# Performance work log

Measured on AMD Instinct MI355X. Metric: run time of the kernel, lower is better.

The kernel has to match this reference:

```python
import jax, jax.numpy as jnp
import numpy as np

N = 50000   # nodes
E = 400000  # edges
G = 256     # graphs in batch
D = 256     # out_dim (scalar channel width)
VD = 16     # vector channel width after v_emb


def setup_inputs() -> dict:
    key = jax.random.key(0)
    ks = jax.random.split(key, 12)

    def rn(k, shape, scale=0.02):
        return (jax.random.normal(k, shape) * scale).astype(jnp.float32)

    return dict(
        node_s=jax.random.normal(ks[0], (N, 23), jnp.float32),
        node_v=jax.random.normal(ks[1], (N, 4, 3), jnp.float32),
        edge_s=jax.random.normal(ks[2], (E, 17), jnp.float32),
        edge_index=jax.random.randint(ks[3], (2, E), 0, N, jnp.int32),
        batch=jnp.sort(jax.random.randint(ks[4], (N,), 0, G, jnp.int32)),
        Ws=rn(ks[5], (23, D)), bs=jnp.zeros((D,), jnp.float32),
        Wv=rn(ks[6], (4, VD)), bv=jnp.zeros((VD,), jnp.float32),
        We=rn(ks[7], (18, D)), be=jnp.zeros((D,), jnp.float32),
        Wm1=rn(ks[8], (2 * D + VD + D, D)), bm1=jnp.zeros((D,), jnp.float32),
        Wm2=rn(ks[9], (D, D)), bm2=jnp.zeros((D,), jnp.float32),
        Wn=rn(ks[10], (D + VD, D)), bn=jnp.zeros((D,), jnp.float32),
        gamma=jnp.ones((D,), jnp.float32), beta=jnp.zeros((D,), jnp.float32),
    )


def reference(node_s, node_v, edge_s, edge_index, batch,
              Ws, bs, Wv, bv, We, be, Wm1, bm1, Wm2, bm2, Wn, bn, gamma, beta):
    # --- embeddings ---
    s = node_s @ Ws + bs                                            # [N, D]
    e_in = jnp.concatenate([edge_s, jnp.zeros((edge_s.shape[0], 1), edge_s.dtype)], axis=-1)  # no edge_v branch
    e = e_in @ We + be                                              # [E, D]
    # v_emb: Linear over the 4 vector channels -> [N, VD, 3]
    v = jnp.einsum('nkc,ko->noc', node_v, Wv) + bv[None, :, None]
    v_norm = jnp.linalg.norm(v, axis=-1)                            # [N, VD]

    # --- SimpleGVPConv: gather -> 2-layer MLP per edge -> scatter-mean ---
    src, dst = edge_index[0], edge_index[1]                         # PyG: s_j = s[src], s_i = s[dst]
    m_in = jnp.concatenate([s[dst], s[src], v_norm[src], e], axis=-1)  # [E, 2D+VD+D]
    m = jax.nn.relu(m_in @ Wm1 + bm1) @ Wm2 + bm2                   # [E, D]
    agg = jax.ops.segment_sum(m, dst, num_segments=N)               # [N, D]
    cnt = jax.ops.segment_sum(jnp.ones((E,), m.dtype), dst, num_segments=N)
    s = s + agg / jnp.maximum(cnt, 1.0)[:, None]                    # mean aggr + residual update

    # --- node MLP: Linear -> LayerNorm -> ReLU (dropout = eval identity) ---
    feat = jnp.concatenate([s, v_norm], axis=-1)                    # [N, D+VD]
    h = feat @ Wn + bn                                              # [N, D]
    mu = h.mean(axis=-1, keepdims=True)
    var = h.var(axis=-1, keepdims=True)
    h = (h - mu) * jax.lax.rsqrt(var + 1e-5) * gamma + beta
    h = jax.nn.relu(h)

    # --- global mean pool ---
    gsum = jax.ops.segment_sum(h, batch, num_segments=G)            # [G, D]
    gcnt = jax.ops.segment_sum(jnp.ones((h.shape[0],), h.dtype), batch, num_segments=G)
    return gsum / jnp.maximum(gcnt, 1.0)[:, None]
```

## Files before the change

kernel.cpp:

```cpp
#include <hip/hip_runtime.h>
#include <hip/hip_bf16.h>

typedef unsigned short u16;
typedef __attribute__((ext_vector_type(8))) short short8;
typedef __attribute__((ext_vector_type(4))) short short4v;
typedef __attribute__((ext_vector_type(4))) float f32x4;

#define NN 50000
#define EE 400000
#define GG 256
#define MP 50048
#define KS 64
#define K2 320
#define EWS 260
#define EAGB 4096
#define NSEG 32
#define SEGSZ 1563

static __device__ __forceinline__ __hip_bfloat16 f2b(float x) { return __float2bfloat16(x); }
static __device__ __forceinline__ float u16tof(u16 v) {
    unsigned x = ((unsigned)v) << 16;
    float f;
    __builtin_memcpy(&f, &x, 4);
    return f;
}
static __device__ __forceinline__ u16 ftou16(float x) {
    __hip_bfloat16 h = __float2bfloat16(x);
    u16 b;
    __builtin_memcpy(&b, &h, 2);
    return b;
}

static __device__ __forceinline__ float dot256(const float* __restrict__ a,
                                               const float* __restrict__ b, int c) {
    const float* __restrict__ bp = b + c;
    float s0 = 0.f, s1 = 0.f, s2 = 0.f, s3 = 0.f;
    float s4 = 0.f, s5 = 0.f, s6 = 0.f, s7 = 0.f;
#pragma unroll 4
    for (int j = 0; j < 256; j += 8) {
        s0 += a[j]     * bp[(size_t)(j)     * 256];
        s1 += a[j + 1] * bp[(size_t)(j + 1) * 256];
        s2 += a[j + 2] * bp[(size_t)(j + 2) * 256];
        s3 += a[j + 3] * bp[(size_t)(j + 3) * 256];
        s4 += a[j + 4] * bp[(size_t)(j + 4) * 256];
        s5 += a[j + 5] * bp[(size_t)(j + 5) * 256];
        s6 += a[j + 6] * bp[(size_t)(j + 6) * 256];
        s7 += a[j + 7] * bp[(size_t)(j + 7) * 256];
    }
    return ((s0 + s1) + (s2 + s3)) + ((s4 + s5) + (s6 + s7));
}

__global__ __launch_bounds__(256) void phase1(const float* __restrict__ Wm1,
                                              const float* __restrict__ Wn,
                                              const float* __restrict__ Wm2,
                                              const float* __restrict__ We,
                                              const float* __restrict__ be,
                                              const float* __restrict__ bm1,
                                              const float* __restrict__ bm2,
                                              const float* __restrict__ Ws,
                                              const float* __restrict__ bs,
                                              __hip_bfloat16* __restrict__ W1pqT,
                                              __hip_bfloat16* __restrict__ W2T,
                                              float* __restrict__ Wc, float* __restrict__ bc,
                                              float* __restrict__ crow,
                                              const float* __restrict__ node_s,
                                              const float* __restrict__ node_v,
                                              const float* __restrict__ Wv,
                                              const float* __restrict__ bv,
                                              __hip_bfloat16* __restrict__ XL2,
                                              const int* __restrict__ ei,
                                              const int* __restrict__ batch,
                                              int* __restrict__ cnt,
                                              int* __restrict__ gstart) {
    int blk = blockIdx.x, tid = threadIdx.x;
    if (blk < 4) {
        int c0 = blk * 128;
        int w = tid >> 6, lane = tid & 63;
        int quad = lane >> 4, l16 = lane & 15;
        f32x4 acc[4][2] = {};
        for (int jt = 0; jt < 256; jt += 32) {
            int j0 = jt + quad * 8;
            short8 af[4], bf[2];
#pragma unroll
            for (int mi = 0; mi < 4; ++mi) {
                int k = mi * 16 + l16;
                const float* ar = nullptr;
                if (k < 23) ar = Ws + (size_t)k * 256;
                else if (k == 39) ar = bs;
                float v0 = 0.f, v1 = 0.f, v2 = 0.f, v3 = 0.f, v4 = 0.f, v5 = 0.f, v6 = 0.f, v7 = 0.f;
                if (ar) {
                    f32x4 x0 = *(const f32x4*)(ar + j0);
                    f32x4 x1 = *(const f32x4*)(ar + j0 + 4);
                    v0 = x0[0]; v1 = x0[1]; v2 = x0[2]; v3 = x0[3];
                    v4 = x1[0]; v5 = x1[1]; v6 = x1[2]; v7 = x1[3];
                }
                af[mi][0] = (short)ftou16(v0); af[mi][1] = (short)ftou16(v1);
                af[mi][2] = (short)ftou16(v2); af[mi][3] = (short)ftou16(v3);
                af[mi][4] = (short)ftou16(v4); af[mi][5] = (short)ftou16(v5);
                af[mi][6] = (short)ftou16(v6); af[mi][7] = (short)ftou16(v7);
            }
#pragma unroll
            for (int ni = 0; ni < 2; ++ni) {
                int c = c0 + w * 32 + ni * 16 + l16;
                const float* Wm1h = (c < 256) ? Wm1 : (Wm1 + 256 * 256);
                int cc = c & 255;
#pragma unroll
                for (int u = 0; u < 8; ++u)
                    bf[ni][u] = (short)ftou16(Wm1h[(size_t)(j0 + u) * 256 + cc]);
            }
#pragma unroll
            for (int mi = 0; mi < 4; ++mi) {
#pragma unroll
                for (int ni = 0; ni < 2; ++ni)
                    acc[mi][ni] = __builtin_amdgcn_mfma_f32_16x16x32_bf16(af[mi], bf[ni], acc[mi][ni], 0, 0, 0);
            }
        }
#pragma unroll
        for (int mi = 0; mi < 4; ++mi) {
#pragma unroll
            for (int ni = 0; ni < 2; ++ni) {
                int c = c0 + w * 32 + ni * 16 + l16;
#pragma unroll
                for (int r = 0; r < 4; ++r) {
                    int k = mi * 16 + quad * 4 + r;
                    float v = acc[mi][ni][r];
                    if (k >= 23 && k < 39)
                        v = (c >= 256) ? Wm1[(size_t)(512 + (k - 23)) * 256 + (c & 255)] : 0.f;
                    W1pqT[(size_t)c * KS + k] = f2b(v);
                }
            }
        }
    } else if (blk < 14) {
        int wb = blk - 4;
        int kt0 = (wb >> 1) * 64;
        int c0 = (wb & 1) * 128;
        int w = tid >> 6, lane = tid & 63;
        int quad = lane >> 4, l16 = lane & 15;
        f32x4 acc[4][2] = {};
        for (int jt = 0; jt < 256; jt += 32) {
            int j0 = jt + quad * 8;
            short8 af[4], bf[2];
#pragma unroll
            for (int mi = 0; mi < 4; ++mi) {
                int k = kt0 + mi * 16 + l16;
                const float* ar = nullptr;
                if (k < 23) ar = Ws + (size_t)k * 256;
                else if (k == 39) ar = bs;
                else if (k >= 40 && k < 296) ar = Wm2 + (size_t)(k - 40) * 256;
                float v0 = 0.f, v1 = 0.f, v2 = 0.f, v3 = 0.f, v4 = 0.f, v5 = 0.f, v6 = 0.f, v7 = 0.f;
                if (ar) {
                    f32x4 x0 = *(const f32x4*)(ar + j0);
                    f32x4 x1 = *(const f32x4*)(ar + j0 + 4);
                    v0 = x0[0]; v1 = x0[1]; v2 = x0[2]; v3 = x0[3];
                    v4 = x1[0]; v5 = x1[1]; v6 = x1[2]; v7 = x1[3];
                }
                af[mi][0] = (short)ftou16(v0); af[mi][1] = (short)ftou16(v1);
                af[mi][2] = (short)ftou16(v2); af[mi][3] = (short)ftou16(v3);
                af[mi][4] = (short)ftou16(v4); af[mi][5] = (short)ftou16(v5);
                af[mi][6] = (short)ftou16(v6); af[mi][7] = (short)ftou16(v7);
            }
#pragma unroll
            for (int ni = 0; ni < 2; ++ni) {
                int c = c0 + w * 32 + ni * 16 + l16;
#pragma unroll
                for (int u = 0; u < 8; ++u)
                    bf[ni][u] = (short)ftou16(Wn[(size_t)(j0 + u) * 256 + c]);
            }
#pragma unroll
            for (int mi = 0; mi < 4; ++mi) {
#pragma unroll
                for (int ni = 0; ni < 2; ++ni)
                    acc[mi][ni] = __builtin_amdgcn_mfma_f32_16x16x32_bf16(af[mi], bf[ni], acc[mi][ni], 0, 0, 0);
            }
        }
#pragma unroll
        for (int mi = 0; mi < 4; ++mi) {
#pragma unroll
            for (int ni = 0; ni < 2; ++ni) {
                int c = c0 + w * 32 + ni * 16 + l16;
#pragma unroll
                for (int r = 0; r < 4; ++r) {
                    int k = kt0 + mi * 16 + quad * 4 + r;
                    float v = acc[mi][ni][r];
                    if (k >= 23 && k < 39) v = Wn[(size_t)(256 + k - 23) * 256 + c];
                    W2T[(size_t)c * K2 + k] = f2b(v);
                }
            }
        }
    } else if (blk < 33) {
        int b = blk - 14, c = tid;
        if (b < 17) Wc[b * 256 + c] = dot256(&We[b * 256], &Wm1[528 * 256], c);
        else if (b == 17) bc[c] = bm1[c] + dot256(be, &Wm1[528 * 256], c);
        else crow[c] = dot256(bm2, Wn, c);
    } else if (blk < 12533) {
        int w = tid >> 6, lane = tid & 63;
        int n = (blk - 33) * 4 + w;
        if (n < NN) {
            float lv = (lane < 23) ? node_s[(size_t)n * 23 + lane] : 0.f;
            float vv = (lane < 12) ? node_v[(size_t)n * 12 + lane] : 0.f;
            float nvk[12];
#pragma unroll
            for (int k = 0; k < 12; ++k) nvk[k] = __shfl(vv, k, 64);
            float vn = 0.f;
            if (lane < 16) {
                float b0 = bv[lane];
                float vx = b0, vy = b0, vz = b0;
#pragma unroll
                for (int k = 0; k < 4; ++k) {
                    float wv = Wv[k * 16 + lane];
                    vx += nvk[k * 3 + 0] * wv;
                    vy += nvk[k * 3 + 1] * wv;
                    vz += nvk[k * 3 + 2] * wv;
                }
                vn = sqrtf(vx * vx + vy * vy + vz * vz);
            }
            int vsrc = (lane >= 23 && lane < 39) ? (lane - 23) : 0;
            float vbc = __shfl(vn, vsrc, 64);
            float outv;
            if (lane < 23) outv = lv;
            else if (lane < 39) outv = vbc;
            else if (lane == 39) outv = 1.f;
            else outv = 0.f;
            __hip_bfloat16* row = XL2 + (size_t)n * K2;
            row[lane] = f2b(outv);
            if (lane < 24) row[296 + lane] = f2b(0.f);
        }
    } else if (blk < 14096) {
        int e = (blk - 12533) * 256 + tid;
        if (e < EE) atomicAdd(&cnt[ei[EE + e]], 1);
    } else {
        int n = (blk - 14096) * 256 + tid;
        if (n < NN) {
            int bn = batch[n];
            int bp = (n == 0) ? -1 : batch[n - 1];
            for (int g = bp + 1; g <= bn; ++g) gstart[g] = n;
            if (n == NN - 1)
                for (int g = bn + 1; g <= GG; ++g) gstart[g] = NN;
        }
    }
}

__global__ __launch_bounds__(256) void scan1(const int* __restrict__ cnt, int* __restrict__ rowptr,
                                             int* __restrict__ bsum) {
    int tid = threadIdx.x, i = blockIdx.x * 256 + tid;
    __shared__ int sd[256];
    int v = (i < NN) ? cnt[i] : 0;
    sd[tid] = v;
    __syncthreads();
    for (int off = 1; off < 256; off <<= 1) {
        int t = (tid >= off) ? sd[tid - off] : 0;
        __syncthreads();
        sd[tid] += t;
        __syncthreads();
    }
    if (i < NN) rowptr[i] = sd[tid] - v;
    if (tid == 255) bsum[blockIdx.x] = sd[255];
}
__global__ __launch_bounds__(256) void scan2(int* __restrict__ bsum, const int* __restrict__ gstart,
                                             float* __restrict__ ginv, int* __restrict__ qc) {
    int c = threadIdx.x;
    __shared__ int sd[256];
    int v = (c < 196) ? bsum[c] : 0;
    sd[c] = v;
    __syncthreads();
    for (int off = 1; off < 256; off <<= 1) {
        int t = (c >= off) ? sd[c - off] : 0;
        __syncthreads();
        sd[c] += t;
        __syncthreads();
    }
    if (c < 196) bsum[c] = sd[c] - v;
    ginv[c] = 1.f / fmaxf((float)(gstart[c + 1] - gstart[c]), 1.f);
    if (c < NSEG) qc[c * 64] = c * SEGSZ + (EAGB / NSEG);
}
__global__ __launch_bounds__(256) void scan3(const int* __restrict__ cnt, const int* __restrict__ bsum,
                                             int* __restrict__ rowptr, int* __restrict__ cursor) {
    int i = blockIdx.x * 256 + threadIdx.x;
    if (i < NN) {
        int v = rowptr[i] + bsum[blockIdx.x];
        rowptr[i] = v;
        cursor[i] = v;
        if (i == NN - 1) rowptr[NN] = v + cnt[i];
    }
}

__global__ __launch_bounds__(256, 2) void gemm1_fill(const u16* __restrict__ A, const u16* __restrict__ Bt,
                                                     __hip_bfloat16* __restrict__ C,
                                                     const int* __restrict__ ei, int* __restrict__ cursor,
                                                     int* __restrict__ eid, int* __restrict__ srcv,
                                                     const float* __restrict__ Wc,
                                                     u16* __restrict__ WcBf) {
    __shared__ __align__(16) u16 At[128 * 64];
    __shared__ __align__(16) u16 Bs[128 * 64];
    int blk = blockIdx.x, tid = threadIdx.x;
    if (blk >= 1564) {
        if (blk == 3127) {
            for (int idx = tid; idx < 8192; idx += 256) {
                int ni = idx >> 9;
                int l = (idx >> 3) & 63;
                int j = idx & 7;
                int k = ((l >> 4) << 3) + j;
                int c = ni * 16 + (l & 15);
                float v = (k < 17) ? Wc[k * 256 + c] : 0.f;
                WcBf[idx] = ftou16(v);
            }
            return;
        }
        int e = (blk - 1564) * 256 + tid;
        if (e < EE) {
            int d = ei[EE + e];
            int s = ei[e];
            int pos = atomicAdd(&cursor[d], 1);
            eid[pos] = e;
            srcv[pos] = s;
        }
        return;
    }
    long m0 = (long)(blk >> 2) * 128;
    long n0 = (long)(blk & 3) * 128;
    int wid = tid >> 6, lane = tid & 63;
    int wm = wid >> 1, wn = wid & 1;
    int quad = lane >> 4, l16 = lane & 15;
    f32x4 acc[4][4] = {};
    int r0 = tid >> 3;
    int cc = (tid & 7) * 8;
    const u16* Ab = A + (m0 + r0) * K2 + cc;
    const u16* Bb = Bt + (n0 + r0) * KS + cc;
#pragma unroll
    for (int i = 0; i < 4; ++i) {
        int row = r0 + i * 32;
        __builtin_amdgcn_global_load_lds(
            (const __attribute__((address_space(1))) void*)(Ab + (long)(i * 32) * K2),
            (__attribute__((address_space(3))) void*)(&At[row * 64 + cc]), 16, 0, 0);
    }
#pragma unroll
    for (int i = 0; i < 4; ++i) {
        int row = r0 + i * 32;
        __builtin_amdgcn_global_load_lds(
            (const __attribute__((address_space(1))) void*)(Bb + (long)(i * 32) * KS),
            (__attribute__((address_space(3))) void*)(&Bs[row * 64 + cc]), 16, 0, 0);
    }
    __syncthreads();
#pragma unroll
    for (int kk = 0; kk < 64; kk += 32) {
        short8 af[4], bf[4];
#pragma unroll
        for (int mi = 0; mi < 4; ++mi)
            af[mi] = *(const short8*)&At[(wm * 64 + mi * 16 + l16) * 64 + kk + quad * 8];
#pragma unroll
        for (int ni = 0; ni < 4; ++ni)
            bf[ni] = *(const short8*)&Bs[(wn * 64 + ni * 16 + l16) * 64 + kk + quad * 8];
#pragma unroll
        for (int mi = 0; mi < 4; ++mi) {
#pragma unroll
            for (int ni = 0; ni < 4; ++ni)
                acc[mi][ni] = __builtin_amdgcn_mfma_f32_16x16x32_bf16(af[mi], bf[ni], acc[mi][ni], 0, 0, 0);
        }
    }
#pragma unroll
    for (int mi = 0; mi < 4; ++mi) {
#pragma unroll
        for (int ni = 0; ni < 4; ++ni) {
            long row = m0 + wm * 64 + mi * 16 + quad * 4;
            long col = n0 + wn * 64 + ni * 16 + l16;
#pragma unroll
            for (int r = 0; r < 4; ++r)
                C[(row + r) * 512 + col] = f2b(acc[mi][ni][r]);
        }
    }
}

__global__ __launch_bounds__(64) void edge_agg(const u16* __restrict__ PQ,
                                               const float* __restrict__ edge_s,
                                               const int* __restrict__ srcv,
                                               const int* __restrict__ eid,
                                               const int* __restrict__ rowptr,
                                               const u16* __restrict__ WcBf,
                                               const float* __restrict__ bc,
                                               int* __restrict__ qc,
                                               __hip_bfloat16* __restrict__ XL2) {
    __shared__ __align__(16) u16 EW[16 * EWS];
    int lane = threadIdx.x;
    int l16 = lane & 15, quad = lane >> 4;
    int seg = blockIdx.x & (NSEG - 1);
    int send = seg * SEGSZ + SEGSZ;
    if (send > NN) send = NN;
    int* segc = qc + seg * 64;
    short8 wcf[16];
#pragma unroll
    for (int ni = 0; ni < 16; ++ni)
        wcf[ni] = *(const short8*)&WcBf[ni * 512 + lane * 8];
    f32x4 bc4 = *(const f32x4*)&bc[lane * 4];
    const f32x4 zf = {0.f, 0.f, 0.f, 0.f};
    int n = seg * SEGSZ + (blockIdx.x >> 5);
    int st = rowptr[n], en = rowptr[n + 1];
    int ee = 0, ss = 0;
    {
        int m0 = en - st;
        if (m0 > 64) m0 = 64;
        if (lane < m0) {
            ee = eid[st + lane];
            ss = srcv[st + lane];
        }
    }
    short4v p4 = *(const short4v*)&PQ[(size_t)n * 512 + lane * 4];
    while (true) {
        int nn = 0;
        if (lane == 0) nn = atomicAdd(segc, 1);
        nn = __builtin_amdgcn_readfirstlane(nn);
        int stN = 0, enN = 0, eeN = 0, ssN = 0;
        short4v p4N = {0, 0, 0, 0};
        if (nn < send) {
            stN = rowptr[nn];
            enN = rowptr[nn + 1];
            int mN = enN - stN;
            if (mN > 64) mN = 64;
            if (lane < mN) {
                eeN = eid[stN + lane];
                ssN = srcv[stN + lane];
            }
            p4N = *(const short4v*)&PQ[(size_t)nn * 512 + lane * 4];
        }
        int deg = en - st;
        f32x4 pb;
#pragma unroll
        for (int i = 0; i < 4; ++i) pb[i] = u16tof((u16)p4[i]) + bc4[i];
        f32x4 acc = {0.f, 0.f, 0.f, 0.f};
        for (int base = 0; base < deg; base += 64) {
            int m = deg - base;
            if (m > 64) m = 64;
            int mm1 = m - 1;
            if (base > 0) {
                ee = 0; ss = 0;
                if (lane < m) {
                    ee = eid[st + base + lane];
                    ss = srcv[st + base + lane];
                }
            }
            auto loadQ = [&](int p) {
                int pc = (p < mm1) ? p : mm1;
                int s = __builtin_amdgcn_readlane(ss, pc);
                return *(const short4v*)&PQ[(size_t)s * 512 + 256 + lane * 4];
            };
            int ng = (m + 15) >> 4;
            for (int g = 0; g < ng; ++g) {
                int b16 = g * 16;
                short4v qA0 = loadQ(b16 + 0);
                short4v qA1 = loadQ(b16 + 1);
                short4v qA2 = loadQ(b16 + 2);
                short4v qA3 = loadQ(b16 + 3);
                short4v qA4 = loadQ(b16 + 4);
                short4v qA5 = loadQ(b16 + 5);
                short4v qA6 = loadQ(b16 + 6);
                short4v qA7 = loadQ(b16 + 7);
                int li = b16 + l16;
                if (li > mm1) li = mm1;
                int ev = __shfl(ee, li, 64);
                const float* ep = edge_s + (size_t)ev * 17 + quad * 8;
                float a0 = 0.f, a1 = 0.f, a2 = 0.f, a3 = 0.f, a4 = 0.f, a5 = 0.f, a6 = 0.f, a7 = 0.f;
                if (quad < 2) {
                    a0 = ep[0]; a1 = ep[1]; a2 = ep[2]; a3 = ep[3];
                    a4 = ep[4]; a5 = ep[5]; a6 = ep[6]; a7 = ep[7];
                } else if (quad == 2) {
                    a0 = ep[0];
                }
                short8 af;
                af[0] = (short)ftou16(a0); af[1] = (short)ftou16(a1);
                af[2] = (short)ftou16(a2); af[3] = (short)ftou16(a3);
                af[4] = (short)ftou16(a4); af[5] = (short)ftou16(a5);
                af[6] = (short)ftou16(a6); af[7] = (short)ftou16(a7);
#pragma unroll
                for (int ni = 0; ni < 16; ++ni) {
                    f32x4 ew = __builtin_amdgcn_mfma_f32_16x16x32_bf16(af, wcf[ni], zf, 0, 0, 0);
#pragma unroll
                    for (int r = 0; r < 4; ++r)
                        EW[(quad * 4 + r) * EWS + ni * 16 + l16] = ftou16(ew[r]);
                }
                int mg = m - b16;
                if (mg > 16) mg = 16;
                short4v qB0 = {0, 0, 0, 0}, qB1 = {0, 0, 0, 0}, qB2 = {0, 0, 0, 0}, qB3 = {0, 0, 0, 0};
                short4v qB4 = {0, 0, 0, 0}, qB5 = {0, 0, 0, 0}, qB6 = {0, 0, 0, 0}, qB7 = {0, 0, 0, 0};
                if (mg > 8) {
                    qB0 = loadQ(b16 + 8);
                    qB1 = loadQ(b16 + 9);
                    qB2 = loadQ(b16 + 10);
                    qB3 = loadQ(b16 + 11);
                    qB4 = loadQ(b16 + 12);
                    qB5 = loadQ(b16 + 13);
                    qB6 = loadQ(b16 + 14);
                    qB7 = loadQ(b16 + 15);
                }
#define CONSUME(QQ, c)                                                              \
                {                                                                   \
                    int jj = (c);                                                   \
                    if (jj < mg) {                                                  \
                        short4v ew4 = *(const short4v*)&EW[jj * EWS + lane * 4];    \
                        _Pragma("unroll")                                           \
                        for (int i = 0; i < 4; ++i)                                 \
                            acc[i] += fmaxf(pb[i] + u16tof((u16)QQ[i]) +            \
                                            u16tof((u16)ew4[i]), 0.f);              \
                    }                                                               \
                }
                CONSUME(qA0, 0)  CONSUME(qA1, 1)  CONSUME(qA2, 2)  CONSUME(qA3, 3)
                CONSUME(qA4, 4)  CONSUME(qA5, 5)  CONSUME(qA6, 6)  CONSUME(qA7, 7)
                CONSUME(qB0, 8)  CONSUME(qB1, 9)  CONSUME(qB2, 10) CONSUME(qB3, 11)
                CONSUME(qB4, 12) CONSUME(qB5, 13) CONSUME(qB6, 14) CONSUME(qB7, 15)
#undef CONSUME
            }
        }
        float inv = 1.f / fmaxf((float)deg, 1.f);
        short4v ov;
#pragma unroll
        for (int i = 0; i < 4; ++i) ov[i] = (short)ftou16(acc[i] * inv);
        *(short4v*)&XL2[(size_t)n * K2 + 40 + lane * 4] = ov;
        if (nn >= send) break;
        n = nn;
        st = stN; en = enN;
        ee = eeN; ss = ssN;
        p4 = p4N;
    }
}

__global__ __launch_bounds__(256, 2) void gemm2_lnp(const u16* __restrict__ A, const u16* __restrict__ Bt,
                                                    const int* __restrict__ cnt, const int* __restrict__ batch,
                                                    const float* __restrict__ bn, const float* __restrict__ crow,
                                                    const float* __restrict__ gamma, const float* __restrict__ beta,
                                                    const float* __restrict__ ginv, float* __restrict__ out) {
    __shared__ __align__(16) u16 At[64 * 64];
    __shared__ __align__(16) u16 Bs[256 * 64];
    __shared__ float rsum[4][64], rsum2[4][64];
    __shared__ int sdeg[64], sbatch[64];
    int tid = threadIdx.x;
    long m0 = (long)blockIdx.x * 64;
    int w = tid >> 6, lane = tid & 63;
    int quad = lane >> 4, l16 = lane & 15;
    f32x4 acc[4][4] = {};
    int r0 = tid >> 3;
    int cc = (tid & 7) * 8;
    const u16* Ab = A + (m0 + r0) * K2 + cc;
    const u16* Bb = Bt + (long)r0 * K2 + cc;
    for (int kt = 0; kt < K2; kt += 64) {
#pragma unroll
        for (int i = 0; i < 2; ++i) {
            int row = r0 + i * 32;
            __builtin_amdgcn_global_load_lds(
                (const __attribute__((address_space(1))) void*)(Ab + (long)(i * 32) * K2 + kt),
                (__attribute__((address_space(3))) void*)(&At[row * 64 + cc]), 16, 0, 0);
        }
#pragma unroll
        for (int i = 0; i < 8; ++i) {
            int row = r0 + i * 32;
            __builtin_amdgcn_global_load_lds(
                (const __attribute__((address_space(1))) void*)(Bb + (long)(i * 32) * K2 + kt),
                (__attribute__((address_space(3))) void*)(&Bs[row * 64 + cc]), 16, 0, 0);
        }
        __syncthreads();
#pragma unroll
        for (int kk = 0; kk < 64; kk += 32) {
            short8 af[4], bf[4];
#pragma unroll
            for (int mi = 0; mi < 4; ++mi)
                af[mi] = *(const short8*)&At[(mi * 16 + l16) * 64 + kk + quad * 8];
#pragma unroll
            for (int ni = 0; ni < 4; ++ni)
                bf[ni] = *(const short8*)&Bs[(w * 64 + ni * 16 + l16) * 64 + kk + quad * 8];
#pragma unroll
            for (int mi = 0; mi < 4; ++mi) {
#pragma unroll
                for (int ni = 0; ni < 4; ++ni)
                    acc[mi][ni] = __builtin_amdgcn_mfma_f32_16x16x32_bf16(af[mi], bf[ni], acc[mi][ni], 0, 0, 0);
            }
        }
        __syncthreads();
    }
    if (tid < 64) {
        long n = m0 + tid;
        sdeg[tid] = (n < NN) ? cnt[n] : 0;
        sbatch[tid] = (n < NN) ? batch[n] : -1;
    }
    __syncthreads();
    float bn_l[4], cr_l[4], g_l[4], be_l[4];
#pragma unroll
    for (int ni = 0; ni < 4; ++ni) {
        int col = w * 64 + ni * 16 + l16;
        bn_l[ni] = bn[col];
        cr_l[ni] = crow[col];
        g_l[ni] = gamma[col];
        be_l[ni] = beta[col];
    }
#pragma unroll
    for (int mi = 0; mi < 4; ++mi) {
#pragma unroll
        for (int r = 0; r < 4; ++r) {
            int row = mi * 16 + quad * 4 + r;
            float cr_on = (sdeg[row] > 0) ? 1.f : 0.f;
            float s = 0.f, s2 = 0.f;
#pragma unroll
            for (int ni = 0; ni < 4; ++ni) {
                float xv = acc[mi][ni][r] + bn_l[ni] + cr_on * cr_l[ni];
                acc[mi][ni][r] = xv;
                s += xv;
                s2 += xv * xv;
            }
            s += __shfl_xor(s, 1, 64);  s2 += __shfl_xor(s2, 1, 64);
            s += __shfl_xor(s, 2, 64);  s2 += __shfl_xor(s2, 2, 64);
            s += __shfl_xor(s, 4, 64);  s2 += __shfl_xor(s2, 4, 64);
            s += __shfl_xor(s, 8, 64);  s2 += __shfl_xor(s2, 8, 64);
            if (l16 == 0) { rsum[w][row] = s; rsum2[w][row] = s2; }
        }
    }
    __syncthreads();
    float mu_a[4][4], rs_a[4][4];
#pragma unroll
    for (int mi = 0; mi < 4; ++mi) {
#pragma unroll
        for (int r = 0; r < 4; ++r) {
            int row = mi * 16 + quad * 4 + r;
            float S = rsum[0][row] + rsum[1][row] + rsum[2][row] + rsum[3][row];
            float S2 = rsum2[0][row] + rsum2[1][row] + rsum2[2][row] + rsum2[3][row];
            float mu = S * (1.f / 256.f);
            mu_a[mi][r] = mu;
            rs_a[mi][r] = rsqrtf(S2 * (1.f / 256.f) - mu * mu + 1e-5f);
        }
    }
#pragma unroll
    for (int ni = 0; ni < 4; ++ni) {
        int col = w * 64 + ni * 16 + l16;
        float pacc = 0.f;
        int curg = -1;
#pragma unroll
        for (int mi = 0; mi < 4; ++mi) {
#pragma unroll
            for (int r = 0; r < 4; ++r) {
                int row = mi * 16 + quad * 4 + r;
                int g = sbatch[row];
                float y = (acc[mi][ni][r] - mu_a[mi][r]) * rs_a[mi][r] * g_l[ni] + be_l[ni];
                y = fmaxf(y, 0.f);
                if (g != curg) {
                    if (curg >= 0) atomicAdd(&out[curg * 256 + col], pacc * ginv[curg]);
                    pacc = 0.f;
                    curg = g;
                }
                if (g >= 0) pacc += y;
            }
        }
        if (curg >= 0) atomicAdd(&out[curg * 256 + col], pacc * ginv[curg]);
    }
}

extern "C" void kernel_launch(void* const* d_in, const int* in_sizes, int n_in,
                              void* d_out, int out_size, void* d_ws, size_t ws_size,
                              hipStream_t stream) {
    const float* node_s = (const float*)d_in[0];
    const float* node_v = (const float*)d_in[1];
    const float* edge_s = (const float*)d_in[2];
    const int* ei = (const int*)d_in[3];
    const int* batch = (const int*)d_in[4];
    const float* Ws = (const float*)d_in[5];
    const float* bs = (const float*)d_in[6];
    const float* Wv = (const float*)d_in[7];
    const float* bv = (const float*)d_in[8];
    const float* We = (const float*)d_in[9];
    const float* be = (const float*)d_in[10];
    const float* Wm1 = (const float*)d_in[11];
    const float* bm1 = (const float*)d_in[12];
    const float* Wm2 = (const float*)d_in[13];
    const float* bm2 = (const float*)d_in[14];
    const float* Wn = (const float*)d_in[15];
    const float* bn = (const float*)d_in[16];
    const float* gamma = (const float*)d_in[17];
    const float* beta = (const float*)d_in[18];

    char* ws = (char*)d_ws;
    size_t off = 0;
    auto take = [&](size_t n) {
        void* p = ws + off;
        off = (off + n + 255) & ~(size_t)255;
        return p;
    };
    __hip_bfloat16* XL2 = (__hip_bfloat16*)take((size_t)MP * K2 * 2);
    __hip_bfloat16* PQ = (__hip_bfloat16*)take((size_t)MP * 512 * 2);
    __hip_bfloat16* W1pqT = (__hip_bfloat16*)take(512 * KS * 2);
    __hip_bfloat16* W2T = (__hip_bfloat16*)take(256 * K2 * 2);
    float* Wc = (float*)take(17 * 256 * 4);
    float* bc = (float*)take(256 * 4);
    float* crow = (float*)take(256 * 4);
    u16* WcBf = (u16*)take(16 * 512 * 2);
    int* cnt = (int*)take(NN * 4);
    int* gstart = (int*)take((GG + 1) * 4);
    float* ginv = (float*)take(GG * 4);
    int* rowptr = (int*)take((NN + 1) * 4);
    int* cursor = (int*)take(NN * 4);
    int* eid = (int*)take(EE * 4);
    int* srcv = (int*)take(EE * 4);
    int* bsum = (int*)take(256 * 4);
    int* qc = (int*)take(NSEG * 64 * 4);

    hipMemsetAsync(cnt, 0, NN * 4, stream);
    hipMemsetAsync(d_out, 0, (size_t)out_size * 4, stream);

    phase1<<<14292, 256, 0, stream>>>(Wm1, Wn, Wm2, We, be, bm1, bm2, Ws, bs,
                                      W1pqT, W2T, Wc, bc, crow,
                                      node_s, node_v, Wv, bv, XL2, ei, batch, cnt, gstart);

    scan1<<<196, 256, 0, stream>>>(cnt, rowptr, bsum);
    scan2<<<1, 256, 0, stream>>>(bsum, gstart, ginv, qc);
    scan3<<<196, 256, 0, stream>>>(cnt, bsum, rowptr, cursor);

    gemm1_fill<<<3128, 256, 0, stream>>>((const u16*)XL2, (const u16*)W1pqT, PQ, ei, cursor, eid,
                                         srcv, Wc, WcBf);

    edge_agg<<<EAGB, 64, 0, stream>>>((const u16*)PQ, edge_s, srcv, eid, rowptr, WcBf, bc, qc, XL2);

    gemm2_lnp<<<782, 256, 0, stream>>>((const u16*)XL2, (const u16*)W2T, cnt, batch,
                                       bn, crow, gamma, beta, ginv, (float*)d_out);
}
```

Measured before the change: 293.5 us.

## Process two destination nodes per wave in edge aggregation to overlap gathers

The edge-aggregation kernel now claims two consecutive nodes per atomic work grab, and each wave prefetches row data for both. When both nodes have degree at most 16, all Q-row gathers and edge-feature loads for both nodes are issued before the MFMA and consume phases, so more memory requests are in flight per wave. Higher-degree pairs fall back to the original per-node path, and the initial work-queue offset is doubled to match the two-node stride. This raises register pressure from the 32 extra short4 gather buffers, which may reduce occupancy or cause spills.

After: 313.3 us. 1.07x slower.

```diff
diff --git a/kernel.cpp b/kernel.cpp
--- a/kernel.cpp
+++ b/kernel.cpp
@@ -271,7 +271,7 @@
     }
     if (c < 196) bsum[c] = sd[c] - v;
     ginv[c] = 1.f / fmaxf((float)(gstart[c + 1] - gstart[c]), 1.f);
-    if (c < NSEG) qc[c * 64] = c * SEGSZ + (EAGB / NSEG);
+    if (c < NSEG) qc[c * 64] = c * SEGSZ + 2 * (EAGB / NSEG);
 }
 __global__ __launch_bounds__(256) void scan3(const int* __restrict__ cnt, const int* __restrict__ bsum,
                                              int* __restrict__ rowptr, int* __restrict__ cursor) {
@@ -392,35 +392,43 @@
         wcf[ni] = *(const short8*)&WcBf[ni * 512 + lane * 8];
     f32x4 bc4 = *(const f32x4*)&bc[lane * 4];
     const f32x4 zf = {0.f, 0.f, 0.f, 0.f};
-    int n = seg * SEGSZ + (blockIdx.x >> 5);
-    int st = rowptr[n], en = rowptr[n + 1];
-    int ee = 0, ss = 0;
-    {
-        int m0 = en - st;
-        if (m0 > 64) m0 = 64;
-        if (lane < m0) {
-            ee = eid[st + lane];
-            ss = srcv[st + lane];
-        }
-    }
-    short4v p4 = *(const short4v*)&PQ[(size_t)n * 512 + lane * 4];
-    while (true) {
-        int nn = 0;
-        if (lane == 0) nn = atomicAdd(segc, 1);
-        nn = __builtin_amdgcn_readfirstlane(nn);
-        int stN = 0, enN = 0, eeN = 0, ssN = 0;
-        short4v p4N = {0, 0, 0, 0};
-        if (nn < send) {
-            stN = rowptr[nn];
-            enN = rowptr[nn + 1];
-            int mN = enN - stN;
-            if (mN > 64) mN = 64;
-            if (lane < mN) {
-                eeN = eid[stN + lane];
-                ssN = srcv[stN + lane];
-            }
-            p4N = *(const short4v*)&PQ[(size_t)nn * 512 + lane * 4];
-        }
+
+    auto buildAf = [&](int ee, int mm1) {
+        int li = l16;
+        if (li > mm1) li = mm1;
+        int ev = __shfl(ee, li, 64);
+        const float* ep = edge_s + (size_t)ev * 17 + quad * 8;
+        float a0 = 0.f, a1 = 0.f, a2 = 0.f, a3 = 0.f, a4 = 0.f, a5 = 0.f, a6 = 0.f, a7 = 0.f;
+        if (quad < 2) {
+            a0 = ep[0]; a1 = ep[1]; a2 = ep[2]; a3 = ep[3];
+            a4 = ep[4]; a5 = ep[5]; a6 = ep[6]; a7 = ep[7];
+        } else if (quad == 2) {
+            a0 = ep[0];
+        }
+        short8 af;
+        af[0] = (short)ftou16(a0); af[1] = (short)ftou16(a1);
+        af[2] = (short)ftou16(a2); af[3] = (short)ftou16(a3);
+        af[4] = (short)ftou16(a4); af[5] = (short)ftou16(a5);
+        af[6] = (short)ftou16(a6); af[7] = (short)ftou16(a7);
+        return af;
+    };
+    auto mfmaToEW = [&](short8 af) {
+#pragma unroll
+        for (int ni = 0; ni < 16; ++ni) {
+            f32x4 ew = __builtin_amdgcn_mfma_f32_16x16x32_bf16(af, wcf[ni], zf, 0, 0, 0);
+#pragma unroll
+            for (int r = 0; r < 4; ++r)
+                EW[(quad * 4 + r) * EWS + ni * 16 + l16] = ftou16(ew[r]);
+        }
+    };
+    auto storeN = [&](int n, f32x4 acc, int deg) {
+        float inv = 1.f / fmaxf((float)deg, 1.f);
+        short4v ov;
+#pragma unroll
+        for (int i = 0; i < 4; ++i) ov[i] = (short)ftou16(acc[i] * inv);
+        *(short4v*)&XL2[(size_t)n * K2 + 40 + lane * 4] = ov;
+    };
+    auto processGeneral = [&](int n, int st, int en, int ee, int ss, short4v p4) {
         int deg = en - st;
         f32x4 pb;
 #pragma unroll
@@ -469,13 +477,7 @@
                 af[2] = (short)ftou16(a2); af[3] = (short)ftou16(a3);
                 af[4] = (short)ftou16(a4); af[5] = (short)ftou16(a5);
                 af[6] = (short)ftou16(a6); af[7] = (short)ftou16(a7);
-#pragma unroll
-                for (int ni = 0; ni < 16; ++ni) {
-                    f32x4 ew = __builtin_amdgcn_mfma_f32_16x16x32_bf16(af, wcf[ni], zf, 0, 0, 0);
-#pragma unroll
-                    for (int r = 0; r < 4; ++r)
-                        EW[(quad * 4 + r) * EWS + ni * 16 + l16] = ftou16(ew[r]);
-                }
+                mfmaToEW(af);
                 int mg = m - b16;
                 if (mg > 16) mg = 16;
                 short4v qB0 = {0, 0, 0, 0}, qB1 = {0, 0, 0, 0}, qB2 = {0, 0, 0, 0}, qB3 = {0, 0, 0, 0};
@@ -508,16 +510,156 @@
 #undef CONSUME
             }
         }
-        float inv = 1.f / fmaxf((float)deg, 1.f);
-        short4v ov;
-#pragma unroll
-        for (int i = 0; i < 4; ++i) ov[i] = (short)ftou16(acc[i] * inv);
-        *(short4v*)&XL2[(size_t)n * K2 + 40 + lane * 4] = ov;
-        if (nn >= send) break;
-        n = nn;
-        st = stN; en = enN;
-        ee = eeN; ss = ssN;
-        p4 = p4N;
+        storeN(n, acc, deg);
+    };
+
+    int nA = seg * SEGSZ + 2 * (blockIdx.x >> 5);
+    int nB = nA + 1;
+    bool vB = nB < send;
+    int stA = rowptr[nA], enA = rowptr[nA + 1];
+    int eeA = 0, ssA = 0;
+    {
+        int m0 = enA - stA;
+        if (m0 > 64) m0 = 64;
+        if (lane < m0) {
+            eeA = eid[stA + lane];
+            ssA = srcv[stA + lane];
+        }
+    }
+    short4v p4A = *(const short4v*)&PQ[(size_t)nA * 512 + lane * 4];
+    int stB = 0, enB = 0, eeB = 0, ssB = 0;
+    short4v p4B = {0, 0, 0, 0};
+    if (vB) {
+        stB = rowptr[nB];
+        enB = rowptr[nB + 1];
+        int m0 = enB - stB;
+        if (m0 > 64) m0 = 64;
+        if (lane < m0) {
+            eeB = eid[stB + lane];
+            ssB = srcv[stB + lane];
+        }
+        p4B = *(const short4v*)&PQ[(size_t)nB * 512 + lane * 4];
+    }
+    while (true) {
+        int nnA = 0;
+        if (lane == 0) nnA = atomicAdd(segc, 2);
+        nnA = __builtin_amdgcn_readfirstlane(nnA);
+        int nnB = nnA + 1;
+        int stNA = 0, enNA = 0, eeNA = 0, ssNA = 0;
+        int stNB = 0, enNB = 0, eeNB = 0, ssNB = 0;
+        short4v p4NA = {0, 0, 0, 0}, p4NB = {0, 0, 0, 0};
+        if (nnA < send) {
+            stNA = rowptr[nnA];
+            enNA = rowptr[nnA + 1];
+            int mN = enNA - stNA;
+            if (mN > 64) mN = 64;
+            if (lane < mN) {
+                eeNA = eid[stNA + lane];
+                ssNA = srcv[stNA + lane];
+            }
+            p4NA = *(const short4v*)&PQ[(size_t)nnA * 512 + lane * 4];
+        }
+        if (nnB < send) {
+            stNB = rowptr[nnB];
+            enNB = rowptr[nnB + 1];
+            int mN = enNB - stNB;
+            if (mN > 64) mN = 64;
+            if (lane < mN) {
+                eeNB = eid[stNB + lane];
+                ssNB = srcv[stNB + lane];
+            }
+            p4NB = *(const short4v*)&PQ[(size_t)nnB * 512 + lane * 4];
+        }
+        int degA = enA - stA;
+        int degB = vB ? (enB - stB) : 0;
+        if (degA <= 16 && degB <= 16) {
+            f32x4 pbA, pbB;
+#pragma unroll
+            for (int i = 0; i < 4; ++i) pbA[i] = u16tof((u16)p4A[i]) + bc4[i];
+#pragma unroll
+            for (int i = 0; i < 4; ++i) pbB[i] = u16tof((u16)p4B[i]) + bc4[i];
+            f32x4 accA = {0.f, 0.f, 0.f, 0.f}, accB = {0.f, 0.f, 0.f, 0.f};
+            int mm1A = degA - 1, mm1B = degB - 1;
+            auto loadQA = [&](int p) {
+                int pc = (p < mm1A) ? p : mm1A;
+                int s = __builtin_amdgcn_readlane(ssA, pc);
+                return *(const short4v*)&PQ[(size_t)s * 512 + 256 + lane * 4];
+            };
+            auto loadQB = [&](int p) {
+                int pc = (p < mm1B) ? p : mm1B;
+                int s = __builtin_amdgcn_readlane(ssB, pc);
+                return *(const short4v*)&PQ[(size_t)s * 512 + 256 + lane * 4];
+            };
+            short4v qA0 = {0,0,0,0}, qA1 = {0,0,0,0}, qA2 = {0,0,0,0}, qA3 = {0,0,0,0};
+            short4v qA4 = {0,0,0,0}, qA5 = {0,0,0,0}, qA6 = {0,0,0,0}, qA7 = {0,0,0,0};
+            short4v qA8 = {0,0,0,0}, qA9 = {0,0,0,0}, qA10 = {0,0,0,0}, qA11 = {0,0,0,0};
+            short4v qA12 = {0,0,0,0}, qA13 = {0,0,0,0}, qA14 = {0,0,0,0}, qA15 = {0,0,0,0};
+            short4v qB0 = {0,0,0,0}, qB1 = {0,0,0,0}, qB2 = {0,0,0,0}, qB3 = {0,0,0,0};
+            short4v qB4 = {0,0,0,0}, qB5 = {0,0,0,0}, qB6 = {0,0,0,0}, qB7 = {0,0,0,0};
+            short4v qB8 = {0,0,0,0}, qB9 = {0,0,0,0}, qB10 = {0,0,0,0}, qB11 = {0,0,0,0};
+            short4v qB12 = {0,0,0,0}, qB13 = {0,0,0,0}, qB14 = {0,0,0,0}, qB15 = {0,0,0,0};
+            short8 afA = {}, afB = {};
+            if (degA > 0) {
+                qA0 = loadQA(0); qA1 = loadQA(1); qA2 = loadQA(2); qA3 = loadQA(3);
+                qA4 = loadQA(4); qA5 = loadQA(5); qA6 = loadQA(6); qA7 = loadQA(7);
+                if (degA > 8) {
+                    qA8 = loadQA(8); qA9 = loadQA(9); qA10 = loadQA(10); qA11 = loadQA(11);
+                    qA12 = loadQA(12); qA13 = loadQA(13); qA14 = loadQA(14); qA15 = loadQA(15);
+                }
+                afA = buildAf(eeA, mm1A);
+            }
+            if (degB > 0) {
+                qB0 = loadQB(0); qB1 = loadQB(1); qB2 = loadQB(2); qB3 = loadQB(3);
+                qB4 = loadQB(4); qB5 = loadQB(5); qB6 = loadQB(6); qB7 = loadQB(7);
+                if (degB > 8) {
+                    qB8 = loadQB(8); qB9 = loadQB(9); qB10 = loadQB(10); qB11 = loadQB(11);
+                    qB12 = loadQB(12); qB13 = loadQB(13); qB14 = loadQB(14); qB15 = loadQB(15);
+                }
+                afB = buildAf(eeB, mm1B);
+            }
+#define CONS(ACC, PB, MG, QQ, c)                                                    \
+            {                                                                       \
+                if ((c) < (MG)) {                                                   \
+                    short4v ew4 = *(const short4v*)&EW[(c) * EWS + lane * 4];       \
+                    _Pragma("unroll")                                               \
+                    for (int i = 0; i < 4; ++i)                                     \
+                        ACC[i] += fmaxf(PB[i] + u16tof((u16)QQ[i]) +                \
+                                        u16tof((u16)ew4[i]), 0.f);                  \
+                }                                                                   \
+            }
+            if (degA > 0) {
+                mfmaToEW(afA);
+                CONS(accA, pbA, degA, qA0, 0)  CONS(accA, pbA, degA, qA1, 1)
+                CONS(accA, pbA, degA, qA2, 2)  CONS(accA, pbA, degA, qA3, 3)
+                CONS(accA, pbA, degA, qA4, 4)  CONS(accA, pbA, degA, qA5, 5)
+                CONS(accA, pbA, degA, qA6, 6)  CONS(accA, pbA, degA, qA7, 7)
+                CONS(accA, pbA, degA, qA8, 8)  CONS(accA, pbA, degA, qA9, 9)
+                CONS(accA, pbA, degA, qA10, 10) CONS(accA, pbA, degA, qA11, 11)
+                CONS(accA, pbA, degA, qA12, 12) CONS(accA, pbA, degA, qA13, 13)
+                CONS(accA, pbA, degA, qA14, 14) CONS(accA, pbA, degA, qA15, 15)
+            }
+            if (degB > 0) {
+                mfmaToEW(afB);
+                CONS(accB, pbB, degB, qB0, 0)  CONS(accB, pbB, degB, qB1, 1)
+                CONS(accB, pbB, degB, qB2, 2)  CONS(accB, pbB, degB, qB3, 3)
+                CONS(accB, pbB, degB, qB4, 4)  CONS(accB, pbB, degB, qB5, 5)
+                CONS(accB, pbB, degB, qB6, 6)  CONS(accB, pbB, degB, qB7, 7)
+                CONS(accB, pbB, degB, qB8, 8)  CONS(accB, pbB, degB, qB9, 9)
+                CONS(accB, pbB, degB, qB10, 10) CONS(accB, pbB, degB, qB11, 11)
+                CONS(accB, pbB, degB, qB12, 12) CONS(accB, pbB, degB, qB13, 13)
+                CONS(accB, pbB, degB, qB14, 14) CONS(accB, pbB, degB, qB15, 15)
+            }
+#undef CONS
+            storeN(nA, accA, degA);
+            if (vB) storeN(nB, accB, degB);
+        } else {
+            processGeneral(nA, stA, enA, eeA, ssA, p4A);
+            if (vB) processGeneral(nB, stB, enB, eeB, ssB, p4B);
+        }
+        if (nnA >= send) break;
+        nA = nnA; nB = nnB; vB = nnB < send;
+        stA = stNA; enA = enNA; eeA = eeNA; ssA = ssNA; p4A = p4NA;
+        stB = stNB; enB = enNB; eeB = eeNB; ssB = ssNB; p4B = p4NB;
     }
 }
 
```
